# Kernel optimization log

Hardware: AMD Instinct MI355X
Metric: run time of the kernel (lower is better)

Reference implementation:

```python
import jax, jax.numpy as jnp
import numpy as np
from jax import lax

EPS = 1e-5
DW_TH = 4.0   # threshold in cut_conv3_5_DW
PW_TH = 1e-3  # threshold in cut_conv3_5_PW


def _bn(x, gamma, beta, mean, var):
    # inference-mode batchnorm over channel dim (NCHW)
    scale = (gamma * lax.rsqrt(var + EPS))[None, :, None, None]
    shift = (beta - mean * gamma * lax.rsqrt(var + EPS))[None, :, None, None]
    return x * scale + shift


def _channel_cut(x, th):
    # faithful to max(torch.max(x[m][k]), -torch.min(x[m][k])) == max |x| per (n, c)
    max_obs = jnp.max(jnp.abs(x), axis=(2, 3), keepdims=True)  # [N, C, 1, 1]
    return jnp.where(max_obs < th, jnp.zeros_like(x), x)


def setup_inputs() -> dict:
    key = jax.random.key(0)
    ks = jax.random.split(key, 6)
    N, Cin, Cout, H, W = 32, 256, 512, 56, 56
    x = jax.random.normal(ks[0], (N, Cin, H, W), dtype=jnp.float32)
    dw_w = jax.random.normal(ks[1], (Cin, 1, 3, 3), dtype=jnp.float32) * 0.3
    dw_b = jax.random.normal(ks[2], (Cin,), dtype=jnp.float32) * 0.1
    pw_w = jax.random.normal(ks[3], (Cout, Cin), dtype=jnp.float32) * 0.05
    pw_b = jax.random.normal(ks[4], (Cout,), dtype=jnp.float32) * 0.1
    return {
        "x": x,
        "dw_w": dw_w,
        "dw_b": dw_b,
        "bn1_gamma": jnp.ones((Cin,), jnp.float32) * 2.0,
        "bn1_beta": jnp.zeros((Cin,), jnp.float32),
        "bn1_mean": jnp.zeros((Cin,), jnp.float32),
        "bn1_var": jnp.ones((Cin,), jnp.float32),
        "pw_w": pw_w,
        "pw_b": pw_b,
        "bn2_gamma": jnp.ones((Cout,), jnp.float32),
        "bn2_beta": jnp.zeros((Cout,), jnp.float32),
        "bn2_mean": jnp.zeros((Cout,), jnp.float32),
        "bn2_var": jnp.ones((Cout,), jnp.float32),
    }


def reference(x, dw_w, dw_b, bn1_gamma, bn1_beta, bn1_mean, bn1_var,
              pw_w, pw_b, bn2_gamma, bn2_beta, bn2_mean, bn2_var):
    Cin = x.shape[1]
    # depthwise 3x3 conv, padding=1 (groups == in_channels)
    y = lax.conv_general_dilated(
        x, dw_w, window_strides=(1, 1), padding=((1, 1), (1, 1)),
        dimension_numbers=("NCHW", "OIHW", "NCHW"),
        feature_group_count=Cin,
    ) + dw_b[None, :, None, None]
    y = jax.nn.relu(_bn(y, bn1_gamma, bn1_beta, bn1_mean, bn1_var))
    y = _channel_cut(y, DW_TH)
    # pointwise 1x1 conv as channel GEMM
    z = jnp.einsum("oc,nchw->nohw", pw_w, y) + pw_b[None, :, None, None]
    z = jax.nn.relu(_bn(z, bn2_gamma, bn2_beta, bn2_mean, bn2_var))
    z = _channel_cut(z, PW_TH)
    return z
```

## Files before the change

kernel.cpp:

```cpp
#include <hip/hip_runtime.h>
#include <hip/hip_bf16.h>

#define HH 56
#define WW 56
#define HW 3136
#define CIN 256
#define COUT 512
#define NBATCH 32
#define EPS 1e-5f
#define DW_TH 4.0f
#define PW_TH 1e-3f

#define CG 32
#define CPITCH 508

typedef __attribute__((ext_vector_type(8))) short s16x8;
typedef __attribute__((ext_vector_type(4))) float f32x4;
typedef unsigned int u32;
typedef unsigned short u16;

__device__ __forceinline__ void async_copy16(void* lds, const void* g) {
    __builtin_amdgcn_global_load_lds((const __attribute__((address_space(1))) unsigned int*)g,
                                     (__attribute__((address_space(3))) unsigned int*)lds,
                                     16, 0, 0);
}

__device__ __forceinline__ u16 bf16_bits(float f) {
    __hip_bfloat16 h = __float2bfloat16(f);
    union { __hip_bfloat16 h; u16 u; } cv; cv.h = h; return cv.u;
}

__global__ __launch_bounds__(256) void prep_kernel(
    const float* __restrict__ pww, const float* __restrict__ pwb,
    const float* __restrict__ g2, const float* __restrict__ b2,
    const float* __restrict__ m2, const float* __restrict__ v2,
    u16* __restrict__ wb, float2* __restrict__ scsh,
    u32* __restrict__ omax, u32* __restrict__ dwmax)
{
    const int gid = blockIdx.x * 256 + threadIdx.x;
    const int base = gid * 8;
    const float4 a = *(const float4*)(pww + base);
    const float4 b = *(const float4*)(pww + base + 4);
    union { u16 u[8]; s16x8 v; } pk;
    pk.u[0] = bf16_bits(a.x); pk.u[1] = bf16_bits(a.y);
    pk.u[2] = bf16_bits(a.z); pk.u[3] = bf16_bits(a.w);
    pk.u[4] = bf16_bits(b.x); pk.u[5] = bf16_bits(b.y);
    pk.u[6] = bf16_bits(b.z); pk.u[7] = bf16_bits(b.w);
    *(s16x8*)(wb + base) = pk.v;
    omax[gid] = 0u;
    if (gid < NBATCH * CIN) dwmax[gid] = 0u;
    if (gid < COUT) {
        const float sc = g2[gid] * rsqrtf(v2[gid] + EPS);
        const float sh = fmaf(-m2[gid], sc, b2[gid]) + pwb[gid] * sc;
        scsh[gid] = make_float2(sc, sh);
    }
}

__global__ __launch_bounds__(256) void dw_kernel(
    const float* __restrict__ x, const float* __restrict__ dww, const float* __restrict__ dwb,
    const float* __restrict__ g1, const float* __restrict__ b1,
    const float* __restrict__ m1, const float* __restrict__ v1,
    u16* __restrict__ y, u32* __restrict__ dwmax)
{
    __shared__ float xs[CG * CPITCH];

    const int bid = blockIdx.x;
    const int cg = bid & 7;
    const int hs = (bid >> 3) & 7;
    const int n  = bid >> 6;
    const int t  = threadIdx.x;

    const int g0     = hs * 7 - 1;
    const int gstart = (g0 < 0) ? 0 : g0;
    const int gend   = (hs * 7 + 7 > 55) ? 55 : hs * 7 + 7;
    const int nrows  = gend - gstart + 1;
    const int dst0   = gstart - g0;
    const int cnt4   = nrows * 14;

    if (hs == 0) {
        for (int i = t; i < CG * 14; i += 256) {
            const int c = i / 14, j = i - c * 14;
            *(float4*)&xs[c * CPITCH + j * 4] = make_float4(0.f, 0.f, 0.f, 0.f);
        }
    } else if (hs == 7) {
        for (int i = t; i < CG * 14; i += 256) {
            const int c = i / 14, j = i - c * 14;
            *(float4*)&xs[c * CPITCH + 8 * 56 + j * 4] = make_float4(0.f, 0.f, 0.f, 0.f);
        }
    }

    {
        const float* gbase = x + (size_t)(n * CIN + cg * CG) * HW + gstart * 56;
        const int half = t >> 7;
        const int i4 = t & 127;
        for (int cc = 0; cc < 16; ++cc) {
            const int c = cc * 2 + half;
            if (i4 < cnt4) {
                const float4 v = *(const float4*)(gbase + (size_t)c * HW + i4 * 4);
                *(float4*)&xs[c * CPITCH + dst0 * 56 + i4 * 4] = v;
            }
        }
    }
    __syncthreads();

    const int r = t >> 5;
    const int c = t & 31;
    float vmax = 0.f;
    if (r < 7) {
        const int ch = cg * CG + c;
        const float* wp = dww + ch * 9;
        const float w00 = wp[0], w01 = wp[1], w02 = wp[2];
        const float w10 = wp[3], w11 = wp[4], w12 = wp[5];
        const float w20 = wp[6], w21 = wp[7], w22 = wp[8];
        const float sc = g1[ch] * rsqrtf(v1[ch] + EPS);
        const float sh = fmaf(-m1[ch], sc, b1[ch]) + dwb[ch] * sc;

        const float* rm = &xs[c * CPITCH + r * 56];
        const float* r0 = rm + 56;
        const float* rp = rm + 112;
        const int grow = hs * 7 + r;
        u16* yo = y + (size_t)(n * HW + grow * WW) * CIN + ch;

        float4 cm = *(const float4*)rm;
        float4 c0 = *(const float4*)r0;
        float4 cp = *(const float4*)rp;
        float lm = 0.f, l0 = 0.f, lp = 0.f;

        for (int chk = 0; chk < 14; ++chk) {
            float4 nm, n0, np;
            if (chk < 13) {
                nm = *(const float4*)(rm + 4 * chk + 4);
                n0 = *(const float4*)(r0 + 4 * chk + 4);
                np = *(const float4*)(rp + 4 * chk + 4);
            } else {
                nm = n0 = np = make_float4(0.f, 0.f, 0.f, 0.f);
            }
            float s0 = w00*lm   + w01*cm.x + w02*cm.y
                     + w10*l0   + w11*c0.x + w12*c0.y
                     + w20*lp   + w21*cp.x + w22*cp.y;
            float s1 = w00*cm.x + w01*cm.y + w02*cm.z
                     + w10*c0.x + w11*c0.y + w12*c0.z
                     + w20*cp.x + w21*cp.y + w22*cp.z;
            float s2 = w00*cm.y + w01*cm.z + w02*cm.w
                     + w10*c0.y + w11*c0.z + w12*c0.w
                     + w20*cp.y + w21*cp.z + w22*cp.w;
            float s3 = w00*cm.z + w01*cm.w + w02*nm.x
                     + w10*c0.z + w11*c0.w + w12*n0.x
                     + w20*cp.z + w21*cp.w + w22*np.x;
            const float v0 = fmaxf(fmaf(s0, sc, sh), 0.f);
            const float v1s = fmaxf(fmaf(s1, sc, sh), 0.f);
            const float v2s = fmaxf(fmaf(s2, sc, sh), 0.f);
            const float v3 = fmaxf(fmaf(s3, sc, sh), 0.f);
            vmax = fmaxf(fmaxf(vmax, fmaxf(v0, v1s)), fmaxf(v2s, v3));
            yo[(4 * chk + 0) * CIN] = bf16_bits(v0);
            yo[(4 * chk + 1) * CIN] = bf16_bits(v1s);
            yo[(4 * chk + 2) * CIN] = bf16_bits(v2s);
            yo[(4 * chk + 3) * CIN] = bf16_bits(v3);
            lm = cm.w; l0 = c0.w; lp = cp.w;
            cm = nm; c0 = n0; cp = np;
        }
    }
    vmax = fmaxf(vmax, __shfl_xor(vmax, 32));
    if ((t & 32) == 0)
        atomicMax(&dwmax[n * CIN + cg * CG + c], __float_as_uint(vmax));
}

__global__ __launch_bounds__(64) void dwcut_kernel(const u32* __restrict__ dwmax, u16* __restrict__ y)
{
    const int b = blockIdx.x;
    if (__uint_as_float(dwmax[b]) >= DW_TH) return;
    const int n = b >> 8, c = b & 255;
    for (int hw = threadIdx.x; hw < HW; hw += 64)
        y[(size_t)(n * HW + hw) * CIN + c] = 0;
}

__global__ __launch_bounds__(256) void pw_kernel(
    const u16* __restrict__ y, const u16* __restrict__ wb,
    const float2* __restrict__ scsh,
    float* __restrict__ out, u32* __restrict__ omax)
{
    __shared__ u16 Wt[128 * 32];
    __shared__ u16 Yt[112 * 32];

    const int hwt = blockIdx.x, ot = blockIdx.y, n = blockIdx.z;
    const int t = threadIdx.x;
    const int w = t >> 6;
    const int l = t & 63;
    const int lo = l & 15, hi = l >> 4;

    const int o_blk  = ot * 128;
    const int hw_blk = n * HW + hwt * 112;

    const u16* wg  = wb + (size_t)(o_blk + w * 32 + (l >> 2)) * CIN + (l & 3) * 8;
    const u16* yg  = y  + (size_t)(hw_blk + (l >> 2)) * CIN + (l & 3) * 8;
    char* WtB = (char*)Wt;
    char* YtB = (char*)Yt;

    f32x4 acc[2][7];
#pragma unroll
    for (int s = 0; s < 2; ++s)
#pragma unroll
        for (int j = 0; j < 7; ++j) acc[s][j] = (f32x4){0.f, 0.f, 0.f, 0.f};

    for (int k0 = 0; k0 < CIN; k0 += 32) {
        async_copy16(WtB + (w * 32 + 0) * 64, wg + k0);
        async_copy16(WtB + (w * 32 + 16) * 64, wg + k0 + (size_t)16 * CIN);
        {
            const int j0 = 2 * w;
            async_copy16(YtB + j0 * 16 * 64, yg + k0 + (size_t)(j0 * 16) * CIN);
            if (j0 + 1 < 7)
                async_copy16(YtB + (j0 + 1) * 16 * 64, yg + k0 + (size_t)((j0 + 1) * 16) * CIN);
        }
        __syncthreads();

        s16x8 af[2], bf[7];
#pragma unroll
        for (int s = 0; s < 2; ++s)
            af[s] = *(const s16x8*)(WtB + (w * 32 + s * 16 + lo) * 64 + hi * 16);
#pragma unroll
        for (int j = 0; j < 7; ++j)
            bf[j] = *(const s16x8*)(YtB + (j * 16 + lo) * 64 + hi * 16);
#pragma unroll
        for (int s = 0; s < 2; ++s)
#pragma unroll
            for (int j = 0; j < 7; ++j)
                acc[s][j] = __builtin_amdgcn_mfma_f32_16x16x32_bf16(af[s], bf[j], acc[s][j], 0, 0, 0);
        __syncthreads();
    }

#pragma unroll
    for (int s = 0; s < 2; ++s) {
#pragma unroll
        for (int r = 0; r < 4; ++r) {
            const int o = o_blk + w * 32 + s * 16 + hi * 4 + r;
            const float2 ss = scsh[o];
            float m = 0.f;
            float* op = out + (size_t)(n * COUT + o) * HW + hwt * 112 + lo;
#pragma unroll
            for (int j = 0; j < 7; ++j) {
                const float v = fmaxf(fmaf(acc[s][j][r], ss.x, ss.y), 0.f);
                op[j * 16] = v;
                m = fmaxf(m, v);
            }
            m = fmaxf(m, __shfl_xor(m, 1));
            m = fmaxf(m, __shfl_xor(m, 2));
            m = fmaxf(m, __shfl_xor(m, 4));
            m = fmaxf(m, __shfl_xor(m, 8));
            if (lo == 0) atomicMax(&omax[n * COUT + o], __float_as_uint(m));
        }
    }
}

__global__ __launch_bounds__(256) void pwcut_kernel(const u32* __restrict__ omax, float* __restrict__ out)
{
    const int b = blockIdx.x;
    if (__uint_as_float(omax[b]) >= PW_TH) return;
    float* p = out + (size_t)b * HW;
    for (int i = threadIdx.x; i < HW; i += 256) p[i] = 0.0f;
}

extern "C" void kernel_launch(void* const* d_in, const int* in_sizes, int n_in,
                              void* d_out, int out_size, void* d_ws, size_t ws_size,
                              hipStream_t stream) {
    const float* x   = (const float*)d_in[0];
    const float* dww = (const float*)d_in[1];
    const float* dwb = (const float*)d_in[2];
    const float* g1  = (const float*)d_in[3];
    const float* b1  = (const float*)d_in[4];
    const float* m1  = (const float*)d_in[5];
    const float* v1  = (const float*)d_in[6];
    const float* pww = (const float*)d_in[7];
    const float* pwb = (const float*)d_in[8];
    const float* g2  = (const float*)d_in[9];
    const float* b2  = (const float*)d_in[10];
    const float* m2  = (const float*)d_in[11];
    const float* v2  = (const float*)d_in[12];
    float* out = (float*)d_out;

    u32*    omax  = (u32*)d_ws;
    u32*    dwmax = (u32*)((char*)d_ws + (64 << 10));
    float2* scsh  = (float2*)((char*)d_ws + (96 << 10));
    u16*    wbf   = (u16*)((char*)d_ws + (128 << 10));
    u16*    y     = (u16*)((char*)d_ws + (1 << 20));

    prep_kernel<<<64, 256, 0, stream>>>(pww, pwb, g2, b2, m2, v2, wbf, scsh, omax, dwmax);
    dw_kernel<<<NBATCH * 8 * 8, 256, 0, stream>>>(x, dww, dwb, g1, b1, m1, v1, y, dwmax);
    dwcut_kernel<<<NBATCH * CIN, 64, 0, stream>>>(dwmax, y);
    dim3 gpw(HW / 112, COUT / 128, NBATCH);
    pw_kernel<<<gpw, 256, 0, stream>>>(y, wbf, scsh, out, omax);
    pwcut_kernel<<<NBATCH * COUT, 256, 0, stream>>>(omax, out);
}
```

Measured before the change: 428.3 us.

## Retile pointwise GEMM to 128x128 blocks with 2x2 wave 64x64 subtiles

The pointwise 1x1-conv GEMM block tile grows from 128 output channels x 112 pixels to 128x128. The four waves are rearranged into a 2x2 grid, each computing a 64x64 subtile with 4x4 MFMA accumulators instead of 32x112. This raises MFMA work per LDS fragment read (8 fragment loads per 16 MFMAs instead of 9 per 14) and cuts the hw-tile count from 28 to 25. The last tile is half out of range: row loads are clamped to valid rows and the out-of-range waves skip the epilogue, so some MFMA work is wasted.

New measurement: 451.9 us. 5.5% more time.

```diff
diff --git a/kernel.cpp b/kernel.cpp
--- a/kernel.cpp
+++ b/kernel.cpp
@@ -180,66 +180,69 @@
     float* __restrict__ out, u32* __restrict__ omax)
 {
     __shared__ u16 Wt[128 * 32];
-    __shared__ u16 Yt[112 * 32];
+    __shared__ u16 Yt[128 * 32];
 
     const int hwt = blockIdx.x, ot = blockIdx.y, n = blockIdx.z;
     const int t = threadIdx.x;
     const int w = t >> 6;
     const int l = t & 63;
     const int lo = l & 15, hi = l >> 4;
-
-    const int o_blk  = ot * 128;
-    const int hw_blk = n * HW + hwt * 112;
-
-    const u16* wg  = wb + (size_t)(o_blk + w * 32 + (l >> 2)) * CIN + (l & 3) * 8;
-    const u16* yg  = y  + (size_t)(hw_blk + (l >> 2)) * CIN + (l & 3) * 8;
+    const int wo = (w >> 1) * 64;
+    const int wh = (w & 1) * 64;
+
+    const int o_blk = ot * 128;
+
+    const int srow = w * 32 + (l >> 2);
+    const u16* wg = wb + (size_t)(o_blk + srow) * CIN + (l & 3) * 8;
+    int yr0 = hwt * 128 + srow;       if (yr0 > HW - 1) yr0 = HW - 1;
+    int yr1 = hwt * 128 + srow + 16;  if (yr1 > HW - 1) yr1 = HW - 1;
+    const u16* yg0 = y + (size_t)(n * HW + yr0) * CIN + (l & 3) * 8;
+    const u16* yg1 = y + (size_t)(n * HW + yr1) * CIN + (l & 3) * 8;
     char* WtB = (char*)Wt;
     char* YtB = (char*)Yt;
 
-    f32x4 acc[2][7];
-#pragma unroll
-    for (int s = 0; s < 2; ++s)
-#pragma unroll
-        for (int j = 0; j < 7; ++j) acc[s][j] = (f32x4){0.f, 0.f, 0.f, 0.f};
+    f32x4 acc[4][4];
+#pragma unroll
+    for (int i = 0; i < 4; ++i)
+#pragma unroll
+        for (int j = 0; j < 4; ++j) acc[i][j] = (f32x4){0.f, 0.f, 0.f, 0.f};
 
     for (int k0 = 0; k0 < CIN; k0 += 32) {
-        async_copy16(WtB + (w * 32 + 0) * 64, wg + k0);
+        async_copy16(WtB + (w * 32) * 64,      wg + k0);
         async_copy16(WtB + (w * 32 + 16) * 64, wg + k0 + (size_t)16 * CIN);
-        {
-            const int j0 = 2 * w;
-            async_copy16(YtB + j0 * 16 * 64, yg + k0 + (size_t)(j0 * 16) * CIN);
-            if (j0 + 1 < 7)
-                async_copy16(YtB + (j0 + 1) * 16 * 64, yg + k0 + (size_t)((j0 + 1) * 16) * CIN);
-        }
+        async_copy16(YtB + (w * 32) * 64,      yg0 + k0);
+        async_copy16(YtB + (w * 32 + 16) * 64, yg1 + k0);
         __syncthreads();
 
-        s16x8 af[2], bf[7];
-#pragma unroll
-        for (int s = 0; s < 2; ++s)
-            af[s] = *(const s16x8*)(WtB + (w * 32 + s * 16 + lo) * 64 + hi * 16);
-#pragma unroll
-        for (int j = 0; j < 7; ++j)
-            bf[j] = *(const s16x8*)(YtB + (j * 16 + lo) * 64 + hi * 16);
-#pragma unroll
-        for (int s = 0; s < 2; ++s)
-#pragma unroll
-            for (int j = 0; j < 7; ++j)
-                acc[s][j] = __builtin_amdgcn_mfma_f32_16x16x32_bf16(af[s], bf[j], acc[s][j], 0, 0, 0);
+        s16x8 af[4], bf[4];
+#pragma unroll
+        for (int so = 0; so < 4; ++so)
+            af[so] = *(const s16x8*)(WtB + (wo + so * 16 + lo) * 64 + hi * 16);
+#pragma unroll
+        for (int sj = 0; sj < 4; ++sj)
+            bf[sj] = *(const s16x8*)(YtB + (wh + sj * 16 + lo) * 64 + hi * 16);
+#pragma unroll
+        for (int so = 0; so < 4; ++so)
+#pragma unroll
+            for (int sj = 0; sj < 4; ++sj)
+                acc[so][sj] = __builtin_amdgcn_mfma_f32_16x16x32_bf16(af[so], bf[sj], acc[so][sj], 0, 0, 0);
         __syncthreads();
     }
 
-#pragma unroll
-    for (int s = 0; s < 2; ++s) {
+    if (hwt == 24 && (w & 1)) return;
+
+#pragma unroll
+    for (int so = 0; so < 4; ++so) {
 #pragma unroll
         for (int r = 0; r < 4; ++r) {
-            const int o = o_blk + w * 32 + s * 16 + hi * 4 + r;
+            const int o = o_blk + wo + so * 16 + hi * 4 + r;
             const float2 ss = scsh[o];
             float m = 0.f;
-            float* op = out + (size_t)(n * COUT + o) * HW + hwt * 112 + lo;
-#pragma unroll
-            for (int j = 0; j < 7; ++j) {
-                const float v = fmaxf(fmaf(acc[s][j][r], ss.x, ss.y), 0.f);
-                op[j * 16] = v;
+            float* op = out + (size_t)(n * COUT + o) * HW + hwt * 128 + wh + lo;
+#pragma unroll
+            for (int sj = 0; sj < 4; ++sj) {
+                const float v = fmaxf(fmaf(acc[so][sj][r], ss.x, ss.y), 0.f);
+                op[sj * 16] = v;
                 m = fmaxf(m, v);
             }
             m = fmaxf(m, __shfl_xor(m, 1));
@@ -286,7 +289,7 @@
     prep_kernel<<<64, 256, 0, stream>>>(pww, pwb, g2, b2, m2, v2, wbf, scsh, omax, dwmax);
     dw_kernel<<<NBATCH * 8 * 8, 256, 0, stream>>>(x, dww, dwb, g1, b1, m1, v1, y, dwmax);
     dwcut_kernel<<<NBATCH * CIN, 64, 0, stream>>>(dwmax, y);
-    dim3 gpw(HW / 112, COUT / 128, NBATCH);
+    dim3 gpw(25, COUT / 128, NBATCH);
     pw_kernel<<<gpw, 256, 0, stream>>>(y, wbf, scsh, out, omax);
     pwcut_kernel<<<NBATCH * COUT, 256, 0, stream>>>(omax, out);
 }
```
